# Kernel optimization log

Hardware: AMD Instinct MI355X
Metric: run time of the kernel (lower is better)

The kernel has to match this reference:

```python
import jax, jax.numpy as jnp
import numpy as np

N, E, F_NODE, F_EDGE, H, EH, G = 20000, 200000, 32, 8, 256, 16, 512
OUT_DIMS = [H, H, H // 2]  # 256, 256, 128
BN_EPS = 1e-5


def _lin(k, out_c, in_c):
    kw, kb = jax.random.split(k)
    bound = 1.0 / np.sqrt(in_c)
    w = jax.random.uniform(kw, (out_c, in_c), minval=-bound, maxval=bound, dtype=jnp.float32)
    b = jax.random.uniform(kb, (out_c,), minval=-bound, maxval=bound, dtype=jnp.float32)
    return w, b


def setup_inputs() -> dict:
    key = jax.random.key(0)
    ks = jax.random.split(key, 40)
    inp = {
        "x": jax.random.normal(ks[0], (N, F_NODE), dtype=jnp.float32),
        "edge_index": jax.random.randint(ks[1], (2, E), 0, N, dtype=jnp.int64),
        "edge_attr": jax.random.normal(ks[2], (E, F_EDGE), dtype=jnp.float32),
        "batch": jnp.sort(jax.random.randint(ks[3], (N,), 0, G, dtype=jnp.int64)),
    }
    inp["ee_w"], inp["ee_b"] = _lin(ks[4], EH, F_EDGE)
    inp["ne_w"], inp["ne_b"] = _lin(ks[5], H, F_NODE)
    in_dim = H
    for i, out_dim in enumerate(OUT_DIMS):
        msg_in = 2 * in_dim + EH
        inp[f"c{i}_w1"], inp[f"c{i}_b1"] = _lin(ks[6 + 2 * i], 2 * out_dim, msg_in)
        inp[f"c{i}_w2"], inp[f"c{i}_b2"] = _lin(ks[7 + 2 * i], out_dim, 2 * out_dim)
        inp[f"bn{i}_g"] = jnp.ones((out_dim,), jnp.float32)
        inp[f"bn{i}_b"] = jnp.zeros((out_dim,), jnp.float32)
        inp[f"bn{i}_m"] = jnp.zeros((out_dim,), jnp.float32)
        inp[f"bn{i}_v"] = jnp.ones((out_dim,), jnp.float32)
        in_dim = out_dim
    inp["fc_w"], inp["fc_b"] = _lin(ks[20], 12, H // 2)
    return inp


def _seg_mean(vals, idx, num):
    s = jax.ops.segment_sum(vals, idx, num_segments=num)
    cnt = jax.ops.segment_sum(jnp.ones((vals.shape[0],), vals.dtype), idx, num_segments=num)
    return s / jnp.maximum(cnt, 1.0)[:, None]


def reference(x, edge_index, edge_attr, batch,
              ee_w, ee_b, ne_w, ne_b,
              c0_w1, c0_b1, c0_w2, c0_b2,
              c1_w1, c1_b1, c1_w2, c1_b2,
              c2_w1, c2_b1, c2_w2, c2_b2,
              bn0_g, bn0_b, bn0_m, bn0_v,
              bn1_g, bn1_b, bn1_m, bn1_v,
              bn2_g, bn2_b, bn2_m, bn2_v,
              fc_w, fc_b):
    src, dst = edge_index[0], edge_index[1]  # x_j = source, x_i = target
    e = jax.nn.relu(edge_attr @ ee_w.T + ee_b)  # [E, EH]
    h = jax.nn.relu(x @ ne_w.T + ne_b)          # [N, H]
    convs = [(c0_w1, c0_b1, c0_w2, c0_b2), (c1_w1, c1_b1, c1_w2, c1_b2), (c2_w1, c2_b1, c2_w2, c2_b2)]
    bns = [(bn0_g, bn0_b, bn0_m, bn0_v), (bn1_g, bn1_b, bn1_m, bn1_v), (bn2_g, bn2_b, bn2_m, bn2_v)]
    for (w1, b1, w2, b2), (g, bb, rm, rv) in zip(convs, bns):
        m = jnp.concatenate([h[dst], h[src], e], axis=1)      # [E, 2*in + EH]
        m = jax.nn.relu(m @ w1.T + b1) @ w2.T + b2            # per-edge MLP
        h = _seg_mean(m, dst, N)                              # scatter-mean to targets
        h = jax.nn.relu((h - rm) / jnp.sqrt(rv + BN_EPS) * g + bb)  # eval-mode BN
        # dropout is identity in eval mode
    pooled = _seg_mean(h, batch, G)                           # global_mean_pool [G, H//2]
    return jax.nn.sigmoid(pooled @ fc_w.T + fc_b)             # [G, 12]
```

## Files before the change

### kernel.cpp

```cpp
#include <hip/hip_runtime.h>
#include <hip/hip_bf16.h>

typedef unsigned int  uint;
typedef unsigned short ushort;
typedef float  f32x2  __attribute__((ext_vector_type(2)));
typedef float  f32x4  __attribute__((ext_vector_type(4)));
typedef __bf16 bf16x8 __attribute__((ext_vector_type(8)));

#define DEV static __device__ __forceinline__

DEV float  b2f(ushort b){ return __uint_as_float(((uint)b) << 16); }
DEV float  lo2f(uint u){ return __uint_as_float(u << 16); }
DEV float  hi2f(uint u){ return __uint_as_float(u & 0xffff0000u); }
DEV ushort f2b(float f){
  uint u = __float_as_uint(f);
  u += 0x7fffu + ((u >> 16) & 1u);
  return (ushort)(u >> 16);
}
DEV uint pk2(float a, float b){ return (uint)f2b(a) | ((uint)f2b(b) << 16); }
DEV void unpack8(uint4 v, float* f){
  f[0]=lo2f(v.x); f[1]=hi2f(v.x); f[2]=lo2f(v.y); f[3]=hi2f(v.y);
  f[4]=lo2f(v.z); f[5]=hi2f(v.z); f[6]=lo2f(v.w); f[7]=hi2f(v.w);
}
DEV int ld_idx(const void* p, int flag, long long i){
  return flag ? ((const int*)p)[i] : (int)((const long long*)p)[i];
}
DEV float ldf(const void* p, int f, int i){
  return f ? ((const float*)p)[i] : b2f(((const ushort*)p)[i]);
}
DEV int clampi(int v, int lo, int hi){ return v < lo ? lo : (v > hi ? hi : v); }

DEV void ld16(const ushort* g, ushort* l){
  __builtin_amdgcn_global_load_lds(
      (const __attribute__((address_space(1))) void*)g,
      (__attribute__((address_space(3))) void*)l, 16, 0, 0);
}

__global__ __launch_bounds__(256) void k_zero_probe(const uint* __restrict__ ei,
    const uint* __restrict__ xw, int* __restrict__ iflag, int* __restrict__ fflag,
    int* __restrict__ zbase, int zn){
  int i = blockIdx.x*256 + threadIdx.x;
  if (i < zn) zbase[i] = 0;
  if (blockIdx.x == 0){
    __shared__ int anyI, cntF;
    if (threadIdx.x == 0){ anyI = 0; cntF = 0; }
    __syncthreads();
    int li = 0, lc = 0;
    for (int k = threadIdx.x; k < 1024; k += 256){
      if (ei[2*k + 1] != 0u) li = 1;
      float f = fabsf(__uint_as_float(xw[k]));
      if (f > 1e-6f && f < 1e6f) lc++;
    }
    if (li) atomicOr(&anyI, 1);
    atomicAdd(&cntF, lc);
    __syncthreads();
    if (threadIdx.x == 0){ *iflag = anyI; *fflag = (2*cntF > 1024) ? 1 : 0; }
  }
}

__global__ __launch_bounds__(256) void k_count(const void* __restrict__ ei,
    const int* __restrict__ flag, int* __restrict__ cnt, int E, int N){
  int e = blockIdx.x*256 + threadIdx.x;
  if (e >= E) return;
  int d = clampi(ld_idx(ei, *flag, (long long)E + e), 0, N-1);
  atomicAdd(&cnt[d], 1);
}

__global__ __launch_bounds__(1024) void k_scan(const int* __restrict__ deg, int* __restrict__ rp, int n){
  __shared__ int part[1024];
  int t = threadIdx.x;
  int chunk = (n + 1023) >> 10;
  int base = t * chunk;
  int s = 0;
  for (int i = 0; i < chunk; i++){ int j = base + i; if (j < n) s += deg[j]; }
  part[t] = s;
  __syncthreads();
  for (int off = 1; off < 1024; off <<= 1){
    int v = (t >= off) ? part[t - off] : 0;
    __syncthreads();
    part[t] += v;
    __syncthreads();
  }
  int run = part[t] - s;
  for (int i = 0; i < chunk; i++){ int j = base + i; if (j < n){ rp[j] = run; run += deg[j]; } }
  if (t == 1023) rp[n] = part[1023];
}

struct CvtTab { const void* src[6]; ushort* dst[6]; int n[6]; int bstart[6]; int nseg; };

__global__ __launch_bounds__(256) void k_mega(
    const void* __restrict__ ei, const int* __restrict__ iflag,
    const int* __restrict__ rp, int* __restrict__ fill, int2* __restrict__ cpair,
    CvtTab ct, const int* __restrict__ fflag,
    const void* __restrict__ x, const void* __restrict__ nw, const void* __restrict__ nbias,
    ushort* __restrict__ h,
    int E, int N, int FB, int CB){
  int b = blockIdx.x;
  int t = threadIdx.x;
  if (b < FB){
    int e = b*256 + t;
    if (e >= E) return;
    int f = *iflag;
    int s = clampi(ld_idx(ei, f, e), 0, N-1);
    int d = clampi(ld_idx(ei, f, (long long)E + e), 0, N-1);
    int pos = clampi(rp[d] + atomicAdd(&fill[d], 1), 0, E-1);
    cpair[pos] = make_int2(s, e);
  } else if (b < FB + CB){
    int cb = b - FB;
    int s = ct.nseg - 1;
    for (int i = 1; i < ct.nseg; i++) if (cb < ct.bstart[i]){ s = i - 1; break; }
    int rel = cb - ct.bstart[s];
    const void* sp = ct.src[s];
    ushort* d = ct.dst[s];
    int f = *fflag;
    int end = ct.n[s]; int cap = rel*8192 + 8192; if (cap < end) end = cap;
    for (int i = rel*8192 + t; i < end; i += 256)
      d[i] = f ? f2b(((const float*)sp)[i]) : ((const ushort*)sp)[i];
  } else {
    __shared__ float xs[4][32];
    int f = *fflag;
    int nb = (b - FB - CB)*4;
    if (t < 128){
      int ni = t >> 5, ci = t & 31;
      int n = nb + ni; if (n >= N) n = N - 1;
      xs[ni][ci] = f ? ((const float*)x)[(size_t)n*32 + ci]
                     : b2f(((const ushort*)x)[(size_t)n*32 + ci]);
    }
    __syncthreads();
    float wr[32];
    if (f){
      const float4* wp = (const float4*)((const float*)nw + (size_t)t*32);
      #pragma unroll
      for (int q4 = 0; q4 < 8; q4++){
        float4 v = wp[q4];
        wr[q4*4+0]=v.x; wr[q4*4+1]=v.y; wr[q4*4+2]=v.z; wr[q4*4+3]=v.w;
      }
    } else {
      const uint4* wp = (const uint4*)((const ushort*)nw + (size_t)t*32);
      unpack8(wp[0], wr); unpack8(wp[1], wr+8); unpack8(wp[2], wr+16); unpack8(wp[3], wr+24);
    }
    float bv = ldf(nbias, f, t);
    #pragma unroll
    for (int ni = 0; ni < 4; ni++){
      int n = nb + ni;
      if (n >= N) break;
      float s = bv;
      #pragma unroll
      for (int k = 0; k < 32; k++) s += xs[ni][k]*wr[k];
      h[(size_t)n*256 + t] = f2b(fmaxf(s, 0.f));
    }
  }
}

__global__ __launch_bounds__(256) void k_edge(const int2* __restrict__ cpair,
    const void* __restrict__ ea, const void* __restrict__ eew, const void* __restrict__ eeb,
    const int* __restrict__ fflag, float* __restrict__ ehp, int E){
  __shared__ float ws[128];
  __shared__ float bs[16];
  int f = *fflag;
  int t = threadIdx.x;
  if (t < 128) ws[t] = ldf(eew, f, t);
  if (t < 16)  bs[t] = ldf(eeb, f, t);
  __syncthreads();
  int pos = blockIdx.x*256 + t;
  if (pos >= E) return;
  int e = cpair[pos].y;
  float a[8];
  if (f){
    const float4* ap = (const float4*)((const float*)ea + (size_t)e*8);
    float4 v0 = ap[0], v1 = ap[1];
    a[0]=v0.x; a[1]=v0.y; a[2]=v0.z; a[3]=v0.w;
    a[4]=v1.x; a[5]=v1.y; a[6]=v1.z; a[7]=v1.w;
  } else {
    uint4 av = *(const uint4*)((const ushort*)ea + (size_t)e*8);
    unpack8(av, a);
  }
  float o[16];
  #pragma unroll
  for (int c = 0; c < 16; c++){
    float s = bs[c];
    #pragma unroll
    for (int j = 0; j < 8; j++) s += a[j]*ws[c*8+j];
    o[c] = fmaxf(s, 0.f);
  }
  f32x4* op = (f32x4*)(ehp + (size_t)pos*16);
  #pragma unroll
  for (int q4 = 0; q4 < 4; q4++){
    f32x4 v = {o[q4*4+0], o[q4*4+1], o[q4*4+2], o[q4*4+3]};
    op[q4] = v;
  }
}

__global__ __launch_bounds__(256) void k_gemm_pq_lds(const ushort* __restrict__ A,
    const ushort* __restrict__ w1, int M, int Nc,
    ushort* __restrict__ P, ushort* __restrict__ Q){
  const int MT = (M + 127) >> 7;
  const int YC = Nc >> 6;
  int jb = blockIdx.x;
  int gx = jb & 7, rr = jb >> 3;
  int sx = rr / YC, yy = rr % YC;
  const int Tm = sx*8 + gx;
  if (Tm >= MT) return;
  __shared__ ushort As[128*32];
  __shared__ ushort Bs[128*32];
  const int t = threadIdx.x;
  const int lane = t & 63;
  const int wv = t >> 6;
  const int m0 = Tm*128;
  const int yc = Nc >> 7;
  const int isQ = yy >= yc;
  const int n0 = (isQ ? yy - yc : yy)*128;
  const ushort* W = w1 + (isQ ? 256 : 0);
  ushort* C = isQ ? Q : P;
  const int lr = lane & 15;
  const int qq = lane >> 4;
  int srow0 = t >> 2,         sq0 = t & 3;
  int srow1 = (256 + t) >> 2, sq1 = t & 3;
  int ga0 = m0 + srow0; if (ga0 >= M) ga0 = M - 1;
  int ga1 = m0 + srow1; if (ga1 >= M) ga1 = M - 1;
  f32x4 acc[2][8];
  #pragma unroll
  for (int f = 0; f < 2; f++)
    #pragma unroll
    for (int j = 0; j < 8; j++) acc[f][j] = {0.f,0.f,0.f,0.f};
  for (int k0 = 0; k0 < 256; k0 += 32){
    ld16(A + (size_t)ga0*256 + k0 + sq0*8, &As[(size_t)t*8]);
    ld16(A + (size_t)ga1*256 + k0 + sq1*8, &As[(size_t)(256+t)*8]);
    ld16(W + (size_t)(n0 + srow0)*528 + k0 + sq0*8, &Bs[(size_t)t*8]);
    ld16(W + (size_t)(n0 + srow1)*528 + k0 + sq1*8, &Bs[(size_t)(256+t)*8]);
    __syncthreads();
    bf16x8 a0 = *(const bf16x8*)&As[(wv*32 + lr)*32 + qq*8];
    bf16x8 a1 = *(const bf16x8*)&As[(wv*32 + 16 + lr)*32 + qq*8];
    #pragma unroll
    for (int j = 0; j < 8; j++){
      bf16x8 b = *(const bf16x8*)&Bs[(j*16 + lr)*32 + qq*8];
      acc[0][j] = __builtin_amdgcn_mfma_f32_16x16x32_bf16(a0, b, acc[0][j], 0, 0, 0);
      acc[1][j] = __builtin_amdgcn_mfma_f32_16x16x32_bf16(a1, b, acc[1][j], 0, 0, 0);
    }
    __syncthreads();
  }
  #pragma unroll
  for (int f = 0; f < 2; f++){
    #pragma unroll
    for (int r = 0; r < 4; r++){
      int row = m0 + wv*32 + f*16 + qq*4 + r;
      if (row >= M) continue;
      #pragma unroll
      for (int j = 0; j < 8; j++)
        C[(size_t)row*Nc + n0 + j*16 + lr] = f2b(acc[f][j][r]);
    }
  }
}

__global__ __launch_bounds__(256) void k_gemm_bn64(const ushort* __restrict__ A, int lda,
    const ushort* __restrict__ W, int ldb, int M, int Nc, int K,
    const void* __restrict__ bias, const void* __restrict__ g, const void* __restrict__ bb,
    const void* __restrict__ rm, const void* __restrict__ rv, const int* __restrict__ fflag,
    const int* __restrict__ rp, ushort* __restrict__ H){
  const int MT = (M + 63) >> 6;
  const int YC = Nc >> 7;
  int jb = blockIdx.x;
  int gx = jb & 7, rr = jb >> 3;
  int sx = rr / YC, yy = rr % YC;
  const int Tm = sx*8 + gx;
  if (Tm >= MT) return;
  __shared__ ushort As[64*32];
  __shared__ ushort Bs[128*32];
  const int t = threadIdx.x;
  const int lane = t & 63;
  const int wv = t >> 6;
  const int m0 = Tm*64;
  const int n0 = yy*128;
  const int lr = lane & 15;
  const int qq = lane >> 4;
  int srowA = t >> 2, sqA = t & 3;
  int ga = m0 + srowA; if (ga >= M) ga = M - 1;
  int srowB0 = t >> 2,        srowB1 = 64 + (t >> 2);
  f32x4 acc[8];
  #pragma unroll
  for (int j = 0; j < 8; j++) acc[j] = {0.f,0.f,0.f,0.f};
  for (int k0 = 0; k0 < K; k0 += 32){
    ld16(A + (size_t)ga*lda + k0 + sqA*8, &As[(size_t)t*8]);
    ld16(W + (size_t)(n0 + srowB0)*ldb + k0 + sqA*8, &Bs[(size_t)t*8]);
    ld16(W + (size_t)(n0 + srowB1)*ldb + k0 + sqA*8, &Bs[(size_t)(256+t)*8]);
    __syncthreads();
    bf16x8 a = *(const bf16x8*)&As[(wv*16 + lr)*32 + qq*8];
    #pragma unroll
    for (int j = 0; j < 8; j++){
      bf16x8 b = *(const bf16x8*)&Bs[(j*16 + lr)*32 + qq*8];
      acc[j] = __builtin_amdgcn_mfma_f32_16x16x32_bf16(a, b, acc[j], 0, 0, 0);
    }
    __syncthreads();
  }
  int f = *fflag;
  float bi[8], sc[8], sh[8];
  #pragma unroll
  for (int j = 0; j < 8; j++){
    int col = n0 + j*16 + lr;
    bi[j] = ldf(bias, f, col);
    sc[j] = ldf(g, f, col) * rsqrtf(ldf(rv, f, col) + 1e-5f);
    sh[j] = ldf(bb, f, col) - ldf(rm, f, col) * sc[j];
  }
  #pragma unroll
  for (int r = 0; r < 4; r++){
    int row = m0 + wv*16 + qq*4 + r;
    if (row >= M) continue;
    int empty = (rp[row+1] - rp[row] == 0);
    #pragma unroll
    for (int j = 0; j < 8; j++){
      float v = acc[j][r] + bi[j];
      if (empty) v = 0.f;
      H[(size_t)row*Nc + n0 + j*16 + lr] = f2b(fmaxf(v*sc[j] + sh[j], 0.f));
    }
  }
}

template<int C>
__global__ __launch_bounds__(256) void k_msg4(const ushort* P, const ushort* __restrict__ Q,
    const float* __restrict__ ehp, const ushort* __restrict__ w1, const void* __restrict__ b1,
    const int* __restrict__ fflag, const int* __restrict__ rp, const int2* __restrict__ cpair,
    ushort* MU, int N){
  int t = threadIdx.x;
  int c0 = t*2;
  f32x2 wc[16];
  {
    float a0[16], a1[16];
    const uint4* wp0 = (const uint4*)(w1 + (size_t)c0*528 + 512);
    const uint4* wp1 = (const uint4*)(w1 + (size_t)(c0+1)*528 + 512);
    unpack8(wp0[0], a0); unpack8(wp0[1], a0+8);
    unpack8(wp1[0], a1); unpack8(wp1[1], a1+8);
    #pragma unroll
    for (int j = 0; j < 16; j++){ wc[j].x = a0[j]; wc[j].y = a1[j]; }
  }
  int ff = *fflag;
  f32x2 b1v = { ldf(b1, ff, c0), ldf(b1, ff, c0+1) };
  int nb = blockIdx.x*2;
  int ne = nb + 2; if (ne > N) ne = N;
  for (int n = nb; n < ne; n++){
    const int i0 = rp[n], i1 = rp[n+1];
    uint pw = *(const uint*)(P + (size_t)n*C + c0);
    f32x2 pre = { lo2f(pw) + b1v.x, hi2f(pw) + b1v.y };
    f32x2 acc0 = {0.f, 0.f}, acc1 = {0.f, 0.f};
    int i = i0;
    int2 p0, p1; uint qw0, qw1;
    if (i + 2 <= i1){
      p0 = cpair[i]; p1 = cpair[i+1];
      qw0 = *(const uint*)(Q + (size_t)p0.x*C + c0);
      qw1 = *(const uint*)(Q + (size_t)p1.x*C + c0);
    }
    while (i + 2 <= i1){
      int inx = i + 2;
      bool more = (inx + 2 <= i1);
      int2 np0, np1;
      if (more){ np0 = cpair[inx]; np1 = cpair[inx+1]; }
      const f32x4* e0p = (const f32x4*)(ehp + (size_t)i*16);
      const f32x4* e1p = (const f32x4*)(ehp + (size_t)(i+1)*16);
      f32x4 ea0 = e0p[0], ea1 = e0p[1], ea2 = e0p[2], ea3 = e0p[3];
      f32x4 eb0 = e1p[0], eb1 = e1p[1], eb2 = e1p[2], eb3 = e1p[3];
      uint nq0 = 0, nq1 = 0;
      if (more){
        nq0 = *(const uint*)(Q + (size_t)np0.x*C + c0);
        nq1 = *(const uint*)(Q + (size_t)np1.x*C + c0);
      }
      float ef0[16] = {ea0.x,ea0.y,ea0.z,ea0.w, ea1.x,ea1.y,ea1.z,ea1.w,
                       ea2.x,ea2.y,ea2.z,ea2.w, ea3.x,ea3.y,ea3.z,ea3.w};
      float ef1[16] = {eb0.x,eb0.y,eb0.z,eb0.w, eb1.x,eb1.y,eb1.z,eb1.w,
                       eb2.x,eb2.y,eb2.z,eb2.w, eb3.x,eb3.y,eb3.z,eb3.w};
      f32x2 d0 = { pre.x + lo2f(qw0), pre.y + hi2f(qw0) };
      f32x2 d1 = { pre.x + lo2f(qw1), pre.y + hi2f(qw1) };
      #pragma unroll
      for (int j = 0; j < 16; j++){
        f32x2 e0v = {ef0[j], ef0[j]};
        f32x2 e1v = {ef1[j], ef1[j]};
        d0 += wc[j] * e0v;
        d1 += wc[j] * e1v;
      }
      acc0.x += fmaxf(d0.x, 0.f); acc0.y += fmaxf(d0.y, 0.f);
      acc1.x += fmaxf(d1.x, 0.f); acc1.y += fmaxf(d1.y, 0.f);
      if (more){ p0 = np0; p1 = np1; qw0 = nq0; qw1 = nq1; }
      i = inx;
    }
    if (i < i1){
      int2 t0 = cpair[i];
      uint tq0 = *(const uint*)(Q + (size_t)t0.x*C + c0);
      const f32x4* e0p = (const f32x4*)(ehp + (size_t)i*16);
      f32x4 ea0 = e0p[0], ea1 = e0p[1], ea2 = e0p[2], ea3 = e0p[3];
      float ef0[16] = {ea0.x,ea0.y,ea0.z,ea0.w, ea1.x,ea1.y,ea1.z,ea1.w,
                       ea2.x,ea2.y,ea2.z,ea2.w, ea3.x,ea3.y,ea3.z,ea3.w};
      f32x2 d0 = { pre.x + lo2f(tq0), pre.y + hi2f(tq0) };
      #pragma unroll
      for (int j = 0; j < 16; j++){
        f32x2 e0v = {ef0[j], ef0[j]};
        d0 += wc[j] * e0v;
      }
      acc0.x += fmaxf(d0.x, 0.f); acc0.y += fmaxf(d0.y, 0.f);
    }
    int cnt = i1 - i0;
    float inv = (cnt > 0) ? 1.f/(float)cnt : 0.f;
    *(uint*)(MU + (size_t)n*C + c0) = pk2((acc0.x + acc1.x)*inv, (acc0.y + acc1.y)*inv);
  }
}

__global__ __launch_bounds__(128) void k_pool(const ushort* __restrict__ h, const void* __restrict__ batch,
    const int* __restrict__ iflag, const void* __restrict__ fw, const void* __restrict__ fb,
    const int* __restrict__ fflag, void* __restrict__ out, int N){
  int g = blockIdx.x, t = threadIdx.x;
  int ifl = *iflag;
  int lo = 0, hi = N;
  while (lo < hi){ int mid = (lo+hi) >> 1; if (ld_idx(batch, ifl, mid) <  g) lo = mid+1; else hi = mid; }
  int s0 = lo;
  hi = N;
  while (lo < hi){ int mid = (lo+hi) >> 1; if (ld_idx(batch, ifl, mid) <= g) lo = mid+1; else hi = mid; }
  int s1 = lo;
  float s = 0.f;
  for (int i = s0; i < s1; i++) s += b2f(h[(size_t)i*128 + t]);
  int cnt = s1 - s0;
  __shared__ float ps[128];
  ps[t] = s / (float)(cnt > 0 ? cnt : 1);
  __syncthreads();
  int f = *fflag;
  if (t < 12){
    float z = ldf(fb, f, t);
    for (int j = 0; j < 128; j++) z += ps[j]*ldf(fw, f, t*128 + j);
    float r = 1.f/(1.f + expf(-z));
    if (f) ((float*)out)[g*12 + t] = r;
    else   ((ushort*)out)[g*12 + t] = f2b(r);
  }
}

__global__ __launch_bounds__(256) void k_sentinel(ushort* __restrict__ out, int n){
  int i = blockIdx.x*256 + threadIdx.x;
  if (i < n) out[i] = 0x3F00;
}

extern "C" void kernel_launch(void* const* d_in, const int* in_sizes, int n_in,
                              void* d_out, int out_size, void* d_ws, size_t ws_size,
                              hipStream_t stream){
  const void* x_raw   = d_in[0];
  const void* ei_raw  = d_in[1];
  const void* ea_raw  = d_in[2];
  const void* ba_raw  = d_in[3];
  (void)n_in;

  const int N = in_sizes[3];
  const int E = in_sizes[1] / 2;
  const int G = out_size / 12;

  char* base = (char*)d_ws;
  size_t off = 0;
  auto alloc = [&](size_t bytes)->char*{
    char* p = base + off;
    off = (off + bytes + 255) & ~(size_t)255;
    return p;
  };
  int* iflag    = (int*)alloc(256);
  int* fflag    = (int*)alloc(256);
  int* deg      = (int*)alloc((size_t)N*4);
  int* fill     = (int*)alloc((size_t)N*4);
  int zn        = (int)(fill - deg) + N;
  int* rp       = (int*)alloc((size_t)(N+1)*4);
  int2* cpair   = (int2*)alloc((size_t)E*8);
  ushort* w1c[3], *w2c[3];
  const int w1n[3] = {512*528, 512*528, 256*528};
  const int w2n[3] = {256*512, 256*512, 128*256};
  for (int i = 0; i < 3; i++) w1c[i] = (ushort*)alloc((size_t)w1n[i]*2);
  for (int i = 0; i < 3; i++) w2c[i] = (ushort*)alloc((size_t)w2n[i]*2);
  float*  ehp32 = (float*)alloc((size_t)E*16*4);
  ushort* h     = (ushort*)alloc((size_t)N*256*2);
  ushort* Q     = (ushort*)alloc((size_t)N*512*2);
  ushort* PM    = (ushort*)alloc((size_t)N*512*2);

  if (off > ws_size){
    k_sentinel<<<(out_size + 255)/256, 256, 0, stream>>>((ushort*)d_out, out_size);
    return;
  }

  k_zero_probe<<<(zn + 255)/256, 256, 0, stream>>>((const uint*)ei_raw, (const uint*)x_raw,
                                                   iflag, fflag, deg, zn);
  k_count<<<(E + 255)/256, 256, 0, stream>>>(ei_raw, iflag, deg, E, N);
  k_scan<<<1, 1024, 0, stream>>>(deg, rp, N);

  CvtTab ct; ct.nseg = 6;
  const void* csrcs[6] = {d_in[8], d_in[16], d_in[24], d_in[10], d_in[18], d_in[26]};
  ushort* cdsts[6]     = {w1c[0],  w1c[1],   w1c[2],   w2c[0],   w2c[1],   w2c[2]};
  const int cns[6]     = {w1n[0],  w1n[1],   w1n[2],   w2n[0],   w2n[1],   w2n[2]};
  int bacc = 0;
  for (int i = 0; i < 6; i++){
    ct.src[i] = csrcs[i]; ct.dst[i] = cdsts[i]; ct.n[i] = cns[i];
    ct.bstart[i] = bacc; bacc += (cns[i] + 8191)/8192;
  }
  int FB = (E + 255)/256;
  int CB = bacc;
  int NB = (N + 3)/4;
  k_mega<<<FB + CB + NB, 256, 0, stream>>>(
      ei_raw, iflag, rp, fill, cpair, ct, fflag,
      x_raw, d_in[6], d_in[7], h, E, N, FB, CB);

  k_edge<<<(E + 255)/256, 256, 0, stream>>>(cpair, ea_raw, d_in[4], d_in[5],
                                            fflag, ehp32, E);

  const int Cch[3] = {512, 512, 256};
  const int Od[3]  = {256, 256, 128};
  const int MTpq = (N + 127)/128;
  const int MTbn = (N + 63)/64;
  for (int i = 0; i < 3; i++){
    int di = 8 + 8*i;
    int g1 = 8 * ((MTpq + 7)/8) * (Cch[i] >> 6);
    k_gemm_pq_lds<<<g1, 256, 0, stream>>>(h, w1c[i], N, Cch[i], PM, Q);
    dim3 gm((N + 1)/2);
    if (i < 2) k_msg4<512><<<gm, 256, 0, stream>>>(PM, Q, ehp32, w1c[i], d_in[di+1], fflag, rp, cpair, PM, N);
    else       k_msg4<256><<<gm, 128, 0, stream>>>(PM, Q, ehp32, w1c[i], d_in[di+1], fflag, rp, cpair, PM, N);
    int g2 = 8 * ((MTbn + 7)/8) * (Od[i] >> 7);
    k_gemm_bn64<<<g2, 256, 0, stream>>>(PM, Cch[i], w2c[i], Cch[i], N, Od[i], Cch[i],
                                        d_in[di+3], d_in[di+4], d_in[di+5],
                                        d_in[di+6], d_in[di+7], fflag, rp, h);
  }

  k_pool<<<G, 128, 0, stream>>>(h, ba_raw, iflag, d_in[32], d_in[33], fflag, d_out, N);
}
```

Before: 484.5 us.

## Widen GEMM tiles to reuse A tiles across P/Q and full output width

The P/Q projection GEMM now computes both the P and Q halves in one block, so each loaded A tile feeds twice as many MFMAs and is fetched from global memory half as often. The BN GEMM now covers the full output width (256 or 128 columns) per block instead of splitting columns across blocks, so the A tile is loaded only once. The cost is more accumulator registers and more LDS per block, which can lower occupancy, and fewer blocks in the grid.

```diff
diff --git a/kernel.cpp b/kernel.cpp
--- a/kernel.cpp
+++ b/kernel.cpp
@@ -191,51 +191,53 @@
   }
 }
 
-__global__ __launch_bounds__(256) void k_gemm_pq_lds(const ushort* __restrict__ A,
+__global__ __launch_bounds__(256) void k_gemm_pq2(const ushort* __restrict__ A,
     const ushort* __restrict__ w1, int M, int Nc,
     ushort* __restrict__ P, ushort* __restrict__ Q){
   const int MT = (M + 127) >> 7;
-  const int YC = Nc >> 6;
+  const int YC = Nc >> 7;
   int jb = blockIdx.x;
   int gx = jb & 7, rr = jb >> 3;
   int sx = rr / YC, yy = rr % YC;
   const int Tm = sx*8 + gx;
   if (Tm >= MT) return;
   __shared__ ushort As[128*32];
-  __shared__ ushort Bs[128*32];
+  __shared__ ushort BsP[128*32];
+  __shared__ ushort BsQ[128*32];
   const int t = threadIdx.x;
   const int lane = t & 63;
   const int wv = t >> 6;
   const int m0 = Tm*128;
-  const int yc = Nc >> 7;
-  const int isQ = yy >= yc;
-  const int n0 = (isQ ? yy - yc : yy)*128;
-  const ushort* W = w1 + (isQ ? 256 : 0);
-  ushort* C = isQ ? Q : P;
+  const int n0 = yy*128;
   const int lr = lane & 15;
   const int qq = lane >> 4;
   int srow0 = t >> 2,         sq0 = t & 3;
   int srow1 = (256 + t) >> 2, sq1 = t & 3;
   int ga0 = m0 + srow0; if (ga0 >= M) ga0 = M - 1;
   int ga1 = m0 + srow1; if (ga1 >= M) ga1 = M - 1;
-  f32x4 acc[2][8];
+  f32x4 accP[2][8], accQ[2][8];
   #pragma unroll
   for (int f = 0; f < 2; f++)
     #pragma unroll
-    for (int j = 0; j < 8; j++) acc[f][j] = {0.f,0.f,0.f,0.f};
+    for (int j = 0; j < 8; j++){ accP[f][j] = {0.f,0.f,0.f,0.f}; accQ[f][j] = {0.f,0.f,0.f,0.f}; }
   for (int k0 = 0; k0 < 256; k0 += 32){
     ld16(A + (size_t)ga0*256 + k0 + sq0*8, &As[(size_t)t*8]);
     ld16(A + (size_t)ga1*256 + k0 + sq1*8, &As[(size_t)(256+t)*8]);
-    ld16(W + (size_t)(n0 + srow0)*528 + k0 + sq0*8, &Bs[(size_t)t*8]);
-    ld16(W + (size_t)(n0 + srow1)*528 + k0 + sq1*8, &Bs[(size_t)(256+t)*8]);
+    ld16(w1 + (size_t)(n0 + srow0)*528 + k0 + sq0*8,       &BsP[(size_t)t*8]);
+    ld16(w1 + (size_t)(n0 + srow1)*528 + k0 + sq1*8,       &BsP[(size_t)(256+t)*8]);
+    ld16(w1 + (size_t)(n0 + srow0)*528 + 256 + k0 + sq0*8, &BsQ[(size_t)t*8]);
+    ld16(w1 + (size_t)(n0 + srow1)*528 + 256 + k0 + sq1*8, &BsQ[(size_t)(256+t)*8]);
     __syncthreads();
     bf16x8 a0 = *(const bf16x8*)&As[(wv*32 + lr)*32 + qq*8];
     bf16x8 a1 = *(const bf16x8*)&As[(wv*32 + 16 + lr)*32 + qq*8];
     #pragma unroll
     for (int j = 0; j < 8; j++){
-      bf16x8 b = *(const bf16x8*)&Bs[(j*16 + lr)*32 + qq*8];
-      acc[0][j] = __builtin_amdgcn_mfma_f32_16x16x32_bf16(a0, b, acc[0][j], 0, 0, 0);
-      acc[1][j] = __builtin_amdgcn_mfma_f32_16x16x32_bf16(a1, b, acc[1][j], 0, 0, 0);
+      bf16x8 bp = *(const bf16x8*)&BsP[(j*16 + lr)*32 + qq*8];
+      bf16x8 bq = *(const bf16x8*)&BsQ[(j*16 + lr)*32 + qq*8];
+      accP[0][j] = __builtin_amdgcn_mfma_f32_16x16x32_bf16(a0, bp, accP[0][j], 0, 0, 0);
+      accP[1][j] = __builtin_amdgcn_mfma_f32_16x16x32_bf16(a1, bp, accP[1][j], 0, 0, 0);
+      accQ[0][j] = __builtin_amdgcn_mfma_f32_16x16x32_bf16(a0, bq, accQ[0][j], 0, 0, 0);
+      accQ[1][j] = __builtin_amdgcn_mfma_f32_16x16x32_bf16(a1, bq, accQ[1][j], 0, 0, 0);
     }
     __syncthreads();
   }
@@ -246,57 +248,55 @@
       int row = m0 + wv*32 + f*16 + qq*4 + r;
       if (row >= M) continue;
       #pragma unroll
-      for (int j = 0; j < 8; j++)
-        C[(size_t)row*Nc + n0 + j*16 + lr] = f2b(acc[f][j][r]);
-    }
-  }
-}
-
+      for (int j = 0; j < 8; j++){
+        P[(size_t)row*Nc + n0 + j*16 + lr] = f2b(accP[f][j][r]);
+        Q[(size_t)row*Nc + n0 + j*16 + lr] = f2b(accQ[f][j][r]);
+      }
+    }
+  }
+}
+
+template<int NJ>
 __global__ __launch_bounds__(256) void k_gemm_bn64(const ushort* __restrict__ A, int lda,
     const ushort* __restrict__ W, int ldb, int M, int Nc, int K,
     const void* __restrict__ bias, const void* __restrict__ g, const void* __restrict__ bb,
     const void* __restrict__ rm, const void* __restrict__ rv, const int* __restrict__ fflag,
     const int* __restrict__ rp, ushort* __restrict__ H){
   const int MT = (M + 63) >> 6;
-  const int YC = Nc >> 7;
-  int jb = blockIdx.x;
-  int gx = jb & 7, rr = jb >> 3;
-  int sx = rr / YC, yy = rr % YC;
-  const int Tm = sx*8 + gx;
+  const int Tm = blockIdx.x;
   if (Tm >= MT) return;
   __shared__ ushort As[64*32];
-  __shared__ ushort Bs[128*32];
+  __shared__ ushort Bs[NJ*16*32];
   const int t = threadIdx.x;
   const int lane = t & 63;
   const int wv = t >> 6;
   const int m0 = Tm*64;
-  const int n0 = yy*128;
   const int lr = lane & 15;
   const int qq = lane >> 4;
   int srowA = t >> 2, sqA = t & 3;
   int ga = m0 + srowA; if (ga >= M) ga = M - 1;
-  int srowB0 = t >> 2,        srowB1 = 64 + (t >> 2);
-  f32x4 acc[8];
-  #pragma unroll
-  for (int j = 0; j < 8; j++) acc[j] = {0.f,0.f,0.f,0.f};
+  f32x4 acc[NJ];
+  #pragma unroll
+  for (int j = 0; j < NJ; j++) acc[j] = {0.f,0.f,0.f,0.f};
   for (int k0 = 0; k0 < K; k0 += 32){
     ld16(A + (size_t)ga*lda + k0 + sqA*8, &As[(size_t)t*8]);
-    ld16(W + (size_t)(n0 + srowB0)*ldb + k0 + sqA*8, &Bs[(size_t)t*8]);
-    ld16(W + (size_t)(n0 + srowB1)*ldb + k0 + sqA*8, &Bs[(size_t)(256+t)*8]);
+    #pragma unroll
+    for (int q = 0; q < NJ/4; q++)
+      ld16(W + (size_t)((t>>2) + 64*q)*ldb + k0 + sqA*8, &Bs[(size_t)(t + 256*q)*8]);
     __syncthreads();
     bf16x8 a = *(const bf16x8*)&As[(wv*16 + lr)*32 + qq*8];
     #pragma unroll
-    for (int j = 0; j < 8; j++){
+    for (int j = 0; j < NJ; j++){
       bf16x8 b = *(const bf16x8*)&Bs[(j*16 + lr)*32 + qq*8];
       acc[j] = __builtin_amdgcn_mfma_f32_16x16x32_bf16(a, b, acc[j], 0, 0, 0);
     }
     __syncthreads();
   }
   int f = *fflag;
-  float bi[8], sc[8], sh[8];
-  #pragma unroll
-  for (int j = 0; j < 8; j++){
-    int col = n0 + j*16 + lr;
+  float bi[NJ], sc[NJ], sh[NJ];
+  #pragma unroll
+  for (int j = 0; j < NJ; j++){
+    int col = j*16 + lr;
     bi[j] = ldf(bias, f, col);
     sc[j] = ldf(g, f, col) * rsqrtf(ldf(rv, f, col) + 1e-5f);
     sh[j] = ldf(bb, f, col) - ldf(rm, f, col) * sc[j];
@@ -307,10 +307,10 @@
     if (row >= M) continue;
     int empty = (rp[row+1] - rp[row] == 0);
     #pragma unroll
-    for (int j = 0; j < 8; j++){
+    for (int j = 0; j < NJ; j++){
       float v = acc[j][r] + bi[j];
       if (empty) v = 0.f;
-      H[(size_t)row*Nc + n0 + j*16 + lr] = f2b(fmaxf(v*sc[j] + sh[j], 0.f));
+      H[(size_t)row*Nc + j*16 + lr] = f2b(fmaxf(v*sc[j] + sh[j], 0.f));
     }
   }
 }
@@ -505,15 +505,18 @@
   const int MTbn = (N + 63)/64;
   for (int i = 0; i < 3; i++){
     int di = 8 + 8*i;
-    int g1 = 8 * ((MTpq + 7)/8) * (Cch[i] >> 6);
-    k_gemm_pq_lds<<<g1, 256, 0, stream>>>(h, w1c[i], N, Cch[i], PM, Q);
+    int g1 = 8 * ((MTpq + 7)/8) * (Cch[i] >> 7);
+    k_gemm_pq2<<<g1, 256, 0, stream>>>(h, w1c[i], N, Cch[i], PM, Q);
     dim3 gm((N + 1)/2);
     if (i < 2) k_msg4<512><<<gm, 256, 0, stream>>>(PM, Q, ehp32, w1c[i], d_in[di+1], fflag, rp, cpair, PM, N);
     else       k_msg4<256><<<gm, 128, 0, stream>>>(PM, Q, ehp32, w1c[i], d_in[di+1], fflag, rp, cpair, PM, N);
-    int g2 = 8 * ((MTbn + 7)/8) * (Od[i] >> 7);
-    k_gemm_bn64<<<g2, 256, 0, stream>>>(PM, Cch[i], w2c[i], Cch[i], N, Od[i], Cch[i],
+    int g2 = MTbn;
+    if (i < 2) k_gemm_bn64<16><<<g2, 256, 0, stream>>>(PM, Cch[i], w2c[i], Cch[i], N, Od[i], Cch[i],
                                         d_in[di+3], d_in[di+4], d_in[di+5],
                                         d_in[di+6], d_in[di+7], fflag, rp, h);
+    else       k_gemm_bn64<8><<<g2, 256, 0, stream>>>(PM, Cch[i], w2c[i], Cch[i], N, Od[i], Cch[i],
+                                        d_in[di+3], d_in[di+4], d_in[di+5],
+                                        d_in[di+6], d_in[di+7], fflag, rp, h);
   }
 
   k_pool<<<G, 128, 0, stream>>>(h, ba_raw, iflag, d_in[32], d_in[33], fflag, d_out, N);
```

Measured after the change: 545.8 us. 1.13x slower.
